# Performance work log

Hardware: AMD Instinct MI355X
Metric: run time of the kernel (lower is better)

Reference implementation:

```python
import jax, jax.numpy as jnp
import numpy as np

REP_THR = 0.6
BORDER = 10


def setup_inputs() -> dict:
    key = jax.random.key(0)
    repeatability = jax.random.uniform(key, (8, 1, 2048, 2048), dtype=jnp.float32)
    return {"repeatability": repeatability}


def reference(repeatability):
    # 3x3 max pool, stride 1, pad 1 (torch pads with -inf for max pool)
    local_max = jax.lax.reduce_window(
        repeatability,
        -jnp.inf,
        jax.lax.max,
        window_dimensions=(1, 1, 3, 3),
        window_strides=(1, 1, 1, 1),
        padding=[(0, 0), (0, 0), (1, 1), (1, 1)],
    )
    maxima = (repeatability == local_max) & (repeatability >= REP_THR)
    # border mask: zero out a 10-pixel frame
    B, C, H, W = repeatability.shape
    border = jnp.zeros((H, W), dtype=bool).at[BORDER:-BORDER, BORDER:-BORDER].set(True)
    maxima = maxima & border  # broadcast over (B, C)
    # Original returns maxima.nonzero().t()[2:4] (data-dependent shape);
    # for jit-compatibility we return the dense boolean mask as float32 —
    # the (y, x) indices are exactly the nonzero positions of this mask.
    return maxima.astype(jnp.float32)
```

## Files before the change

kernel.cpp:

```cpp
#include <hip/hip_runtime.h>
#include <math.h>

#define IMG_H 2048
#define IMG_W 2048
#define NB    8
#define BORDER 10
#define REP_THR 0.6f
#define ROWS 8

typedef float f32x4 __attribute__((ext_vector_type(4)));

__global__ __launch_bounds__(256) void nms_kernel(const float* __restrict__ in,
                                                  float* __restrict__ out) {
    const int tid = blockIdx.x * blockDim.x + threadIdx.x;
    const int gx  = tid & 511;
    const int gys = (tid >> 9) & 255;
    const int b   = tid >> 17;

    const int x4 = gx << 2;
    const int y0 = gys << 3;

    const size_t img_off = (size_t)b * IMG_H * IMG_W;
    float* obase = out + img_off + (size_t)y0 * IMG_W + x4;

    if (gx == 0 || gx == 511 || y0 + ROWS <= BORDER || y0 >= IMG_H - BORDER) {
        const f32x4 z = {0.f, 0.f, 0.f, 0.f};
#pragma unroll
        for (int j = 0; j < ROWS; ++j)
            __builtin_nontemporal_store(z, (f32x4*)(obase + (size_t)j * IMG_W));
        return;
    }

    const float* ibase = in + img_off + x4;

    f32x4 v[ROWS + 2];
    float l[ROWS + 2], q[ROWS + 2];
#pragma unroll
    for (int r = 0; r < ROWS + 2; ++r) {
        int rc = y0 - 1 + r;
        rc = rc < (BORDER - 1) ? (BORDER - 1)
           : (rc > (IMG_H - BORDER) ? (IMG_H - BORDER) : rc);
        const float* row = ibase + (size_t)rc * IMG_W;
        v[r] = *(const f32x4*)row;
        l[r] = row[-1];
        q[r] = row[4];
    }

    f32x4 h[ROWS + 2];
#pragma unroll
    for (int r = 0; r < ROWS + 2; ++r) {
        h[r][0] = fmaxf(l[r],    fmaxf(v[r][0], v[r][1]));
        h[r][1] = fmaxf(v[r][0], fmaxf(v[r][1], v[r][2]));
        h[r][2] = fmaxf(v[r][1], fmaxf(v[r][2], v[r][3]));
        h[r][3] = fmaxf(v[r][2], fmaxf(v[r][3], q[r]));
    }

    const bool bx0 = (x4 + 0 >= BORDER) && (x4 + 0 < IMG_W - BORDER);
    const bool bx1 = (x4 + 1 >= BORDER) && (x4 + 1 < IMG_W - BORDER);
    const bool bx2 = (x4 + 2 >= BORDER) && (x4 + 2 < IMG_W - BORDER);
    const bool bx3 = (x4 + 3 >= BORDER) && (x4 + 3 < IMG_W - BORDER);

#pragma unroll
    for (int j = 0; j < ROWS; ++j) {
        const int y = y0 + j;
        const bool rowok = (y >= BORDER) && (y < IMG_H - BORDER);

        f32x4 m;
        m[0] = fmaxf(h[j][0], fmaxf(h[j + 1][0], h[j + 2][0]));
        m[1] = fmaxf(h[j][1], fmaxf(h[j + 1][1], h[j + 2][1]));
        m[2] = fmaxf(h[j][2], fmaxf(h[j + 1][2], h[j + 2][2]));
        m[3] = fmaxf(h[j][3], fmaxf(h[j + 1][3], h[j + 2][3]));

        const f32x4 c = v[j + 1];
        f32x4 r;
        r[0] = (c[0] == m[0] && c[0] >= REP_THR && bx0 && rowok) ? 1.f : 0.f;
        r[1] = (c[1] == m[1] && c[1] >= REP_THR && bx1 && rowok) ? 1.f : 0.f;
        r[2] = (c[2] == m[2] && c[2] >= REP_THR && bx2 && rowok) ? 1.f : 0.f;
        r[3] = (c[3] == m[3] && c[3] >= REP_THR && bx3 && rowok) ? 1.f : 0.f;

        __builtin_nontemporal_store(r, (f32x4*)(obase + (size_t)j * IMG_W));
    }
}

extern "C" void kernel_launch(void* const* d_in, const int* in_sizes, int n_in,
                              void* d_out, int out_size, void* d_ws, size_t ws_size,
                              hipStream_t stream) {
    const float* in = (const float*)d_in[0];
    float* out = (float*)d_out;
    const int total_threads = NB * (IMG_H / ROWS) * (IMG_W / 4);
    const int block = 256;
    const int grid = total_threads / block;
    nms_kernel<<<grid, block, 0, stream>>>(in, out);
}
```

Measured before the change: 230.1 us.

## Stage full-width row slabs in LDS via direct global-to-LDS loads

```diff
diff --git a/kernel.cpp b/kernel.cpp
--- a/kernel.cpp
+++ b/kernel.cpp
@@ -1,84 +1,98 @@
 #include <hip/hip_runtime.h>
 #include <math.h>
+#include <stdint.h>
 
 #define IMG_H 2048
 #define IMG_W 2048
 #define NB    8
 #define BORDER 10
 #define REP_THR 0.6f
-#define ROWS 8
+#define ROWS  6
+#define SROWS (ROWS + 2)
+#define SLABS 342
 
 typedef float f32x4 __attribute__((ext_vector_type(4)));
 
 __global__ __launch_bounds__(256) void nms_kernel(const float* __restrict__ in,
                                                   float* __restrict__ out) {
-    const int tid = blockIdx.x * blockDim.x + threadIdx.x;
-    const int gx  = tid & 511;
-    const int gys = (tid >> 9) & 255;
-    const int b   = tid >> 17;
+    __shared__ float tile[SROWS][IMG_W];
 
-    const int x4 = gx << 2;
-    const int y0 = gys << 3;
+    const int nwg  = NB * SLABS;
+    const int orig = blockIdx.x;
+    const int swz  = (orig & 7) * (nwg >> 3) + (orig >> 3);
+    const int b    = swz / SLABS;
+    const int slab = swz % SLABS;
+    const int y0   = slab * ROWS;
+
+    const int t    = threadIdx.x;
+    const int lane = t & 63;
+    const int wave = t >> 6;
 
     const size_t img_off = (size_t)b * IMG_H * IMG_W;
-    float* obase = out + img_off + (size_t)y0 * IMG_W + x4;
-
-    if (gx == 0 || gx == 511 || y0 + ROWS <= BORDER || y0 >= IMG_H - BORDER) {
-        const f32x4 z = {0.f, 0.f, 0.f, 0.f};
-#pragma unroll
-        for (int j = 0; j < ROWS; ++j)
-            __builtin_nontemporal_store(z, (f32x4*)(obase + (size_t)j * IMG_W));
-        return;
-    }
-
-    const float* ibase = in + img_off + x4;
-
-    f32x4 v[ROWS + 2];
-    float l[ROWS + 2], q[ROWS + 2];
-#pragma unroll
-    for (int r = 0; r < ROWS + 2; ++r) {
-        int rc = y0 - 1 + r;
-        rc = rc < (BORDER - 1) ? (BORDER - 1)
-           : (rc > (IMG_H - BORDER) ? (IMG_H - BORDER) : rc);
-        const float* row = ibase + (size_t)rc * IMG_W;
-        v[r] = *(const f32x4*)row;
-        l[r] = row[-1];
-        q[r] = row[4];
-    }
-
-    f32x4 h[ROWS + 2];
-#pragma unroll
-    for (int r = 0; r < ROWS + 2; ++r) {
-        h[r][0] = fmaxf(l[r],    fmaxf(v[r][0], v[r][1]));
-        h[r][1] = fmaxf(v[r][0], fmaxf(v[r][1], v[r][2]));
-        h[r][2] = fmaxf(v[r][1], fmaxf(v[r][2], v[r][3]));
-        h[r][3] = fmaxf(v[r][2], fmaxf(v[r][3], q[r]));
-    }
-
-    const bool bx0 = (x4 + 0 >= BORDER) && (x4 + 0 < IMG_W - BORDER);
-    const bool bx1 = (x4 + 1 >= BORDER) && (x4 + 1 < IMG_W - BORDER);
-    const bool bx2 = (x4 + 2 >= BORDER) && (x4 + 2 < IMG_W - BORDER);
-    const bool bx3 = (x4 + 3 >= BORDER) && (x4 + 3 < IMG_W - BORDER);
+    const float* ibase = in + img_off;
 
 #pragma unroll
-    for (int j = 0; j < ROWS; ++j) {
-        const int y = y0 + j;
-        const bool rowok = (y >= BORDER) && (y < IMG_H - BORDER);
+    for (int i = 0; i < 16; ++i) {
+        const int k = wave * 16 + i;
+        const int r = k >> 3;
+        const int cc = k & 7;
+        int g = y0 - 1 + r;
+        g = g < (BORDER - 1) ? (BORDER - 1)
+          : (g > (IMG_H - BORDER) ? (IMG_H - BORDER) : g);
+        const float* src = ibase + (size_t)g * IMG_W + (cc << 8) + (lane << 2);
+        float* dst = &tile[r][cc << 8];
+        __builtin_amdgcn_global_load_lds(
+            (const __attribute__((address_space(1))) void*)src,
+            (__attribute__((address_space(3))) void*)dst,
+            16, 0, 0);
+    }
+    __syncthreads();
 
-        f32x4 m;
-        m[0] = fmaxf(h[j][0], fmaxf(h[j + 1][0], h[j + 2][0]));
-        m[1] = fmaxf(h[j][1], fmaxf(h[j + 1][1], h[j + 2][1]));
-        m[2] = fmaxf(h[j][2], fmaxf(h[j + 1][2], h[j + 2][2]));
-        m[3] = fmaxf(h[j][3], fmaxf(h[j + 1][3], h[j + 2][3]));
+#pragma unroll
+    for (int p = 0; p < 2; ++p) {
+        const int c0 = (t << 2) + (p << 10);
+        const int cl = (c0 == 0) ? 0 : c0 - 1;
+        const int cr = (c0 + 4 < IMG_W) ? c0 + 4 : IMG_W - 1;
+        f32x4 v[SROWS], h[SROWS];
+#pragma unroll
+        for (int r = 0; r < SROWS; ++r) {
+            v[r] = *(const f32x4*)&tile[r][c0];
+            const float l = tile[r][cl];
+            const float q = tile[r][cr];
+            h[r][0] = fmaxf(l,       fmaxf(v[r][0], v[r][1]));
+            h[r][1] = fmaxf(v[r][0], fmaxf(v[r][1], v[r][2]));
+            h[r][2] = fmaxf(v[r][1], fmaxf(v[r][2], v[r][3]));
+            h[r][3] = fmaxf(v[r][2], fmaxf(v[r][3], q));
+        }
 
-        const f32x4 c = v[j + 1];
-        f32x4 r;
-        r[0] = (c[0] == m[0] && c[0] >= REP_THR && bx0 && rowok) ? 1.f : 0.f;
-        r[1] = (c[1] == m[1] && c[1] >= REP_THR && bx1 && rowok) ? 1.f : 0.f;
-        r[2] = (c[2] == m[2] && c[2] >= REP_THR && bx2 && rowok) ? 1.f : 0.f;
-        r[3] = (c[3] == m[3] && c[3] >= REP_THR && bx3 && rowok) ? 1.f : 0.f;
+        const bool bx0 = (c0 + 0 >= BORDER) && (c0 + 0 < IMG_W - BORDER);
+        const bool bx1 = (c0 + 1 >= BORDER) && (c0 + 1 < IMG_W - BORDER);
+        const bool bx2 = (c0 + 2 >= BORDER) && (c0 + 2 < IMG_W - BORDER);
+        const bool bx3 = (c0 + 3 >= BORDER) && (c0 + 3 < IMG_W - BORDER);
 
-        __builtin_nontemporal_store(r, (f32x4*)(obase + (size_t)j * IMG_W));
+        float* obase = out + img_off + (size_t)y0 * IMG_W + c0;
+#pragma unroll
+        for (int j = 0; j < ROWS; ++j) {
+            const int y = y0 + j;
+            if (y < IMG_H) {
+                const bool rowok = (y >= BORDER) && (y < IMG_H - BORDER);
+
+                f32x4 m;
+                m[0] = fmaxf(h[j][0], fmaxf(h[j + 1][0], h[j + 2][0]));
+                m[1] = fmaxf(h[j][1], fmaxf(h[j + 1][1], h[j + 2][1]));
+                m[2] = fmaxf(h[j][2], fmaxf(h[j + 1][2], h[j + 2][2]));
+                m[3] = fmaxf(h[j][3], fmaxf(h[j + 1][3], h[j + 2][3]));
+
+                const f32x4 c = v[j + 1];
+                f32x4 r;
+                r[0] = (c[0] == m[0] && c[0] >= REP_THR && bx0 && rowok) ? 1.f : 0.f;
+                r[1] = (c[1] == m[1] && c[1] >= REP_THR && bx1 && rowok) ? 1.f : 0.f;
+                r[2] = (c[2] == m[2] && c[2] >= REP_THR && bx2 && rowok) ? 1.f : 0.f;
+                r[3] = (c[3] == m[3] && c[3] >= REP_THR && bx3 && rowok) ? 1.f : 0.f;
+
+                __builtin_nontemporal_store(r, (f32x4*)(obase + (size_t)j * IMG_W));
+            }
+        }
     }
 }
 
@@ -87,8 +101,6 @@
                               hipStream_t stream) {
     const float* in = (const float*)d_in[0];
     float* out = (float*)d_out;
-    const int total_threads = NB * (IMG_H / ROWS) * (IMG_W / 4);
-    const int block = 256;
-    const int grid = total_threads / block;
-    nms_kernel<<<grid, block, 0, stream>>>(in, out);
+    const int grid = NB * SLABS;
+    nms_kernel<<<grid, 256, 0, stream>>>(in, out);
 }
```

Result: slower. 235.4 us (+2.3%).

## Process one row per thread and swizzle blocks across XCDs

Applied to the files above, without the earlier changes.

```diff
diff --git a/kernel.cpp b/kernel.cpp
--- a/kernel.cpp
+++ b/kernel.cpp
@@ -6,80 +6,74 @@
 #define NB    8
 #define BORDER 10
 #define REP_THR 0.6f
-#define ROWS 8
 
 typedef float f32x4 __attribute__((ext_vector_type(4)));
 
 __global__ __launch_bounds__(256) void nms_kernel(const float* __restrict__ in,
                                                   float* __restrict__ out) {
-    const int tid = blockIdx.x * blockDim.x + threadIdx.x;
-    const int gx  = tid & 511;
-    const int gys = (tid >> 9) & 255;
-    const int b   = tid >> 17;
+    const int orig = blockIdx.x;
+    const int swz  = (orig & 7) * 4096 + (orig >> 3);
+    const int tid  = (swz << 8) | threadIdx.x;
+
+    const int gx = tid & 511;
+    const int y  = (tid >> 9) & 2047;
+    const int b  = tid >> 20;
 
     const int x4 = gx << 2;
-    const int y0 = gys << 3;
 
     const size_t img_off = (size_t)b * IMG_H * IMG_W;
-    float* obase = out + img_off + (size_t)y0 * IMG_W + x4;
+    float* optr = out + img_off + (size_t)y * IMG_W + x4;
 
-    if (gx == 0 || gx == 511 || y0 + ROWS <= BORDER || y0 >= IMG_H - BORDER) {
+    if (y < BORDER || y >= IMG_H - BORDER || gx == 0 || gx == 511) {
         const f32x4 z = {0.f, 0.f, 0.f, 0.f};
-#pragma unroll
-        for (int j = 0; j < ROWS; ++j)
-            __builtin_nontemporal_store(z, (f32x4*)(obase + (size_t)j * IMG_W));
+        __builtin_nontemporal_store(z, (f32x4*)optr);
         return;
     }
 
-    const float* ibase = in + img_off + x4;
+    const float* base = in + img_off + (size_t)y * IMG_W + x4;
+    const float* r0 = base - IMG_W;
+    const float* r1 = base;
+    const float* r2 = base + IMG_W;
 
-    f32x4 v[ROWS + 2];
-    float l[ROWS + 2], q[ROWS + 2];
-#pragma unroll
-    for (int r = 0; r < ROWS + 2; ++r) {
-        int rc = y0 - 1 + r;
-        rc = rc < (BORDER - 1) ? (BORDER - 1)
-           : (rc > (IMG_H - BORDER) ? (IMG_H - BORDER) : rc);
-        const float* row = ibase + (size_t)rc * IMG_W;
-        v[r] = *(const f32x4*)row;
-        l[r] = row[-1];
-        q[r] = row[4];
-    }
+    const f32x4 v0 = *(const f32x4*)r0;
+    const f32x4 v1 = *(const f32x4*)r1;
+    const f32x4 v2 = *(const f32x4*)r2;
+    const float l0 = r0[-1], q0 = r0[4];
+    const float l1 = r1[-1], q1 = r1[4];
+    const float l2 = r2[-1], q2 = r2[4];
 
-    f32x4 h[ROWS + 2];
-#pragma unroll
-    for (int r = 0; r < ROWS + 2; ++r) {
-        h[r][0] = fmaxf(l[r],    fmaxf(v[r][0], v[r][1]));
-        h[r][1] = fmaxf(v[r][0], fmaxf(v[r][1], v[r][2]));
-        h[r][2] = fmaxf(v[r][1], fmaxf(v[r][2], v[r][3]));
-        h[r][3] = fmaxf(v[r][2], fmaxf(v[r][3], q[r]));
-    }
+    f32x4 h0, h1, h2;
+    h0[0] = fmaxf(l0,    fmaxf(v0[0], v0[1]));
+    h0[1] = fmaxf(v0[0], fmaxf(v0[1], v0[2]));
+    h0[2] = fmaxf(v0[1], fmaxf(v0[2], v0[3]));
+    h0[3] = fmaxf(v0[2], fmaxf(v0[3], q0));
+    h1[0] = fmaxf(l1,    fmaxf(v1[0], v1[1]));
+    h1[1] = fmaxf(v1[0], fmaxf(v1[1], v1[2]));
+    h1[2] = fmaxf(v1[1], fmaxf(v1[2], v1[3]));
+    h1[3] = fmaxf(v1[2], fmaxf(v1[3], q1));
+    h2[0] = fmaxf(l2,    fmaxf(v2[0], v2[1]));
+    h2[1] = fmaxf(v2[0], fmaxf(v2[1], v2[2]));
+    h2[2] = fmaxf(v2[1], fmaxf(v2[2], v2[3]));
+    h2[3] = fmaxf(v2[2], fmaxf(v2[3], q2));
+
+    f32x4 m;
+    m[0] = fmaxf(h0[0], fmaxf(h1[0], h2[0]));
+    m[1] = fmaxf(h0[1], fmaxf(h1[1], h2[1]));
+    m[2] = fmaxf(h0[2], fmaxf(h1[2], h2[2]));
+    m[3] = fmaxf(h0[3], fmaxf(h1[3], h2[3]));
 
     const bool bx0 = (x4 + 0 >= BORDER) && (x4 + 0 < IMG_W - BORDER);
     const bool bx1 = (x4 + 1 >= BORDER) && (x4 + 1 < IMG_W - BORDER);
     const bool bx2 = (x4 + 2 >= BORDER) && (x4 + 2 < IMG_W - BORDER);
     const bool bx3 = (x4 + 3 >= BORDER) && (x4 + 3 < IMG_W - BORDER);
 
-#pragma unroll
-    for (int j = 0; j < ROWS; ++j) {
-        const int y = y0 + j;
-        const bool rowok = (y >= BORDER) && (y < IMG_H - BORDER);
+    f32x4 r;
+    r[0] = (v1[0] == m[0] && v1[0] >= REP_THR && bx0) ? 1.f : 0.f;
+    r[1] = (v1[1] == m[1] && v1[1] >= REP_THR && bx1) ? 1.f : 0.f;
+    r[2] = (v1[2] == m[2] && v1[2] >= REP_THR && bx2) ? 1.f : 0.f;
+    r[3] = (v1[3] == m[3] && v1[3] >= REP_THR && bx3) ? 1.f : 0.f;
 
-        f32x4 m;
-        m[0] = fmaxf(h[j][0], fmaxf(h[j + 1][0], h[j + 2][0]));
-        m[1] = fmaxf(h[j][1], fmaxf(h[j + 1][1], h[j + 2][1]));
-        m[2] = fmaxf(h[j][2], fmaxf(h[j + 1][2], h[j + 2][2]));
-        m[3] = fmaxf(h[j][3], fmaxf(h[j + 1][3], h[j + 2][3]));
-
-        const f32x4 c = v[j + 1];
-        f32x4 r;
-        r[0] = (c[0] == m[0] && c[0] >= REP_THR && bx0 && rowok) ? 1.f : 0.f;
-        r[1] = (c[1] == m[1] && c[1] >= REP_THR && bx1 && rowok) ? 1.f : 0.f;
-        r[2] = (c[2] == m[2] && c[2] >= REP_THR && bx2 && rowok) ? 1.f : 0.f;
-        r[3] = (c[3] == m[3] && c[3] >= REP_THR && bx3 && rowok) ? 1.f : 0.f;
-
-        __builtin_nontemporal_store(r, (f32x4*)(obase + (size_t)j * IMG_W));
-    }
+    __builtin_nontemporal_store(r, (f32x4*)optr);
 }
 
 extern "C" void kernel_launch(void* const* d_in, const int* in_sizes, int n_in,
@@ -87,7 +81,7 @@
                               hipStream_t stream) {
     const float* in = (const float*)d_in[0];
     float* out = (float*)d_out;
-    const int total_threads = NB * (IMG_H / ROWS) * (IMG_W / 4);
+    const int total_threads = NB * IMG_H * (IMG_W / 4);
     const int block = 256;
     const int grid = total_threads / block;
     nms_kernel<<<grid, block, 0, stream>>>(in, out);
```

After: 229.7 us. Within noise of the previous version (-0.2%).
